# Optimization experiments

Measured on AMD Instinct MI355X. Metric: run time of the kernel, lower is better.

Reference implementation:

```python
import jax, jax.numpy as jnp
import numpy as np

B, S, H, NH = 2, 2048, 1024, 16
HD = H // NH  # head_dim = 64


def setup_inputs() -> dict:
    key = jax.random.key(0)
    k1, k2, k3, k4, k5 = jax.random.split(key, 5)
    hidden_states = jax.random.normal(k1, (B, S, H), dtype=jnp.float32)
    # additive causal mask: 0 on/below diagonal, -1e9 above
    causal = jnp.tril(jnp.ones((S, S), dtype=jnp.bool_))
    attention_mask = jnp.where(causal, 0.0, -1e9).astype(jnp.float32)[None, None, :, :]
    scale = 0.02
    Wq = jax.random.normal(k2, (H, H), dtype=jnp.float32) * scale
    Wk = jax.random.normal(k3, (H, H), dtype=jnp.float32) * scale
    Wv = jax.random.normal(k4, (H, H), dtype=jnp.float32) * scale
    Wo = jax.random.normal(k5, (H, H), dtype=jnp.float32) * scale
    return {"hidden_states": hidden_states, "attention_mask": attention_mask,
            "Wq": Wq, "Wk": Wk, "Wv": Wv, "Wo": Wo}


def reference(hidden_states, attention_mask, Wq, Wk, Wv, Wo):
    b, s, _ = hidden_states.shape
    # nn.Linear: y = x @ W.T
    q = (hidden_states @ Wq.T).reshape(b, s, NH, HD).transpose(0, 2, 1, 3)  # [B,NH,S,HD]
    k = (hidden_states @ Wk.T).reshape(b, s, NH, HD).transpose(0, 2, 1, 3)
    v = (hidden_states @ Wv.T).reshape(b, s, NH, HD).transpose(0, 2, 1, 3)
    scores = jnp.einsum('bhqd,bhkd->bhqk', q, k) / jnp.sqrt(jnp.float32(HD))
    scores = scores + attention_mask
    attn = jax.nn.softmax(scores, axis=-1)
    out = jnp.einsum('bhqk,bhkd->bhqd', attn, v)  # [B,NH,S,HD]
    out = out.transpose(0, 2, 1, 3).reshape(b, s, H)
    return out @ Wo.T
```

## Files before the change

kernel.cpp:

```cpp
#include <hip/hip_runtime.h>
#include <hip/hip_bf16.h>

#define B_   2
#define S_   2048
#define H_   1024
#define NH_  16
#define HD_  64
#define MTOT 4096
#define KD   1024

typedef __attribute__((ext_vector_type(4)))  float    f32x4;
typedef __attribute__((ext_vector_type(16))) float    f32x16;
typedef __attribute__((ext_vector_type(8)))  short    bf16x8;
typedef __attribute__((ext_vector_type(4)))  short    bf16x4;
typedef __attribute__((ext_vector_type(2)))  unsigned u32x2;
typedef __attribute__((ext_vector_type(4)))  unsigned u32x4;

__device__ inline short f2bf(float x) {
    union { float f; unsigned u; } v; v.f = x;
    unsigned r = v.u + 0x7fffu + ((v.u >> 16) & 1u);
    return (short)(r >> 16);
}
__device__ inline unsigned pk2(float lo, float hi) {
    return (unsigned)(unsigned short)f2bf(lo) | ((unsigned)(unsigned short)f2bf(hi) << 16);
}
__device__ inline unsigned cvtpk(float lo, float hi) {
    unsigned r;
    asm("v_cvt_pk_bf16_f32 %0, %1, %2" : "=v"(r) : "v"(lo), "v"(hi));
    return r;
}
__device__ inline float max3f(float a, float b, float c) {
    float r;
    asm("v_max3_f32 %0, %1, %2, %3" : "=v"(r) : "v"(a), "v"(b), "v"(c));
    return r;
}
__device__ inline void gload16(const void* g, void* l) {
    __builtin_amdgcn_global_load_lds(
        (const __attribute__((address_space(1))) unsigned*)g,
        (__attribute__((address_space(3))) unsigned*)l, 16, 0, 0);
}

__global__ __launch_bounds__(256) void cvt_x(const float* __restrict__ x,
                                             unsigned* __restrict__ xb) {
    const size_t i = ((size_t)blockIdx.x * 256 + threadIdx.x) * 8;
    const f32x4 a = *(const f32x4*)(x + i);
    const f32x4 b = *(const f32x4*)(x + i + 4);
    u32x4 p;
    p[0] = pk2(a[0], a[1]); p[1] = pk2(a[2], a[3]);
    p[2] = pk2(b[0], b[1]); p[3] = pk2(b[2], b[3]);
    *(u32x4*)(xb + i / 2) = p;
}

__global__ __launch_bounds__(256) void wcvt(const float* __restrict__ W0,
                                            const float* __restrict__ W1,
                                            const float* __restrict__ W2,
                                            const float* __restrict__ W3,
                                            unsigned* __restrict__ wb) {
    const float* W = (blockIdx.y == 0) ? W0 : (blockIdx.y == 1) ? W1
                   : (blockIdx.y == 2) ? W2 : W3;
    const size_t i = ((size_t)blockIdx.x * 256 + threadIdx.x) * 8;
    const f32x4 a = *(const f32x4*)(W + i);
    const f32x4 b = *(const f32x4*)(W + i + 4);
    u32x4 p;
    p[0] = pk2(a[0], a[1]); p[1] = pk2(a[2], a[3]);
    p[2] = pk2(b[0], b[1]); p[3] = pk2(b[2], b[3]);
    *(u32x4*)(wb + (size_t)blockIdx.y * (H_ * KD / 2) + i / 2) = p;
}

template <int MODE>
__global__ __launch_bounds__(256) void gemm_m97(const short* __restrict__ A,
                                                const short* __restrict__ Wb,
                                                short* __restrict__ outb,
                                                float* __restrict__ outf) {
    __shared__ short Sm[128 * 128];
    short* As = Sm;
    short* Bs = Sm + 8192;

    const int tid = threadIdx.x, wave = tid >> 6, lane = tid & 63;
    const int wm = (wave >> 1) * 64, wn = (wave & 1) * 64;
    const int m0 = blockIdx.x * 128;

    int n0, widx;
    if constexpr (MODE == 0) {
        widx = blockIdx.y >> 3;
        n0 = (blockIdx.y & 7) * 128;
    } else {
        widx = 0;
        n0 = blockIdx.y * 128;
    }
    const short* W = Wb + (size_t)widx * H_ * KD;

    f32x4 acc[4][4] = {};

    for (int k0 = 0; k0 < KD; k0 += 64) {
#pragma unroll
        for (int c = 0; c < 4; ++c) {
            const int lin = wave * 4096 + c * 1024 + lane * 16;
            const int row = lin >> 7;
            const int col = (lin & 127) ^ ((row & 7) << 4);
            gload16(A + (size_t)(m0 + row) * KD + k0 + (col >> 1),
                    (char*)As + wave * 4096 + c * 1024);
            gload16(W + (size_t)(n0 + row) * KD + k0 + (col >> 1),
                    (char*)Bs + wave * 4096 + c * 1024);
        }
        __syncthreads();

#pragma unroll
        for (int ks = 0; ks < 2; ++ks) {
            bf16x8 af[4], bf[4];
#pragma unroll
            for (int i = 0; i < 4; ++i) {
                const int row = wm + i * 16 + (lane & 15);
                af[i] = *(const bf16x8*)((char*)As + row * 128 +
                        ((ks * 64 + (lane >> 4) * 16) ^ ((row & 7) << 4)));
            }
#pragma unroll
            for (int j = 0; j < 4; ++j) {
                const int row = wn + j * 16 + (lane & 15);
                bf[j] = *(const bf16x8*)((char*)Bs + row * 128 +
                        ((ks * 64 + (lane >> 4) * 16) ^ ((row & 7) << 4)));
            }
#pragma unroll
            for (int i = 0; i < 4; ++i)
#pragma unroll
                for (int j = 0; j < 4; ++j)
                    acc[i][j] = __builtin_amdgcn_mfma_f32_16x16x32_bf16(af[i], bf[j], acc[i][j], 0, 0, 0);
        }
        __syncthreads();
    }

    if constexpr (MODE == 0) {
        if (widx == 2) {
#pragma unroll
            for (int i = 0; i < 4; ++i)
#pragma unroll
                for (int j = 0; j < 4; ++j) {
                    const int mi2 = (wm + i * 16 + (lane >> 4) * 4) * 2;
                    const int ni  = wn + j * 16 + (lane & 15);
                    bf16x4 w;
#pragma unroll
                    for (int r = 0; r < 4; ++r) w[r] = f2bf(acc[i][j][r]);
                    *(bf16x4*)((char*)Sm + ((ni * 256 + mi2) ^ ((ni & 7) << 4))) = w;
                }
            __syncthreads();
            const int d = tid >> 1, shalf = tid & 1;
            const int bb = m0 >> 11, sbase = (m0 & 2047) + shalf * 64;
            const int hd = (n0 + d) >> 6, dd = (n0 + d) & 63;
            short* dst = outb + (size_t)2 * MTOT * H_ +
                         (((size_t)(bb * NH_ + hd)) * HD_ + dd) * S_ + sbase;
#pragma unroll
            for (int k = 0; k < 8; ++k) {
                const int byt = (d * 256 + shalf * 128 + k * 16) ^ ((d & 7) << 4);
                *(bf16x8*)(dst + k * 8) = *(const bf16x8*)((char*)Sm + byt);
            }
        } else {
#pragma unroll
            for (int i = 0; i < 4; ++i)
#pragma unroll
                for (int j = 0; j < 4; ++j)
#pragma unroll
                    for (int r = 0; r < 4; ++r) {
                        const int mi = wm + i * 16 + (lane >> 4) * 4 + r;
                        const int ni = wn + j * 16 + (lane & 15);
                        const int byt = (mi * 256 + ni * 2) ^ ((mi & 7) << 4);
                        *(short*)((char*)Sm + byt) = f2bf(acc[i][j][r]);
                    }
            __syncthreads();
            const int row = tid >> 1, half = tid & 1;
            const int m = m0 + row, bb = m >> 11, s = m & 2047;
            const int hh = (n0 >> 6) + half;
            short* dst = outb + (size_t)widx * MTOT * H_ +
                         (((size_t)(bb * NH_ + hh)) * S_ + s) * HD_;
#pragma unroll
            for (int k = 0; k < 8; ++k) {
                const int byt = (row * 256 + half * 128 + k * 16) ^ ((row & 7) << 4);
                *(bf16x8*)(dst + k * 8) = *(const bf16x8*)((char*)Sm + byt);
            }
        }
    } else {
#pragma unroll
        for (int i = 0; i < 4; ++i)
#pragma unroll
            for (int j = 0; j < 4; ++j)
#pragma unroll
                for (int r = 0; r < 4; ++r) {
                    const int m = m0 + wm + i * 16 + (lane >> 4) * 4 + r;
                    const int n = n0 + wn + j * 16 + (lane & 15);
                    outf[(size_t)m * H_ + n] = acc[i][j][r];
                }
    }
}

__global__ __launch_bounds__(128, 4) void flash8(const short* __restrict__ Qb,
                                                 const short* __restrict__ Kb,
                                                 const short* __restrict__ Vtb,
                                                 short* __restrict__ Ob) {
    const int u = blockIdx.x;
    const int qu = 63 - (u >> 5);
    const int bh = u & 31;
    const int b = bh >> 4, h = bh & 15;

    const int tid = threadIdx.x, par = tid >> 6, lane = tid & 63;
    const int qw0 = qu * 32;
    const size_t hoff = ((size_t)(b * NH_ + h)) * S_ * HD_;
    const short* Q  = Qb  + hoff;
    const short* K  = Kb  + hoff;
    const short* Vt = Vtb + hoff;

    const int ql = lane & 31;
    const int hh = lane >> 5;

    bf16x8 qf[4];
#pragma unroll
    for (int ds = 0; ds < 4; ++ds)
        qf[ds] = *(const bf16x8*)(Q + (size_t)(qw0 + ql) * HD_ + ds * 16 + hh * 8);

    f32x16 ot[2] = {};
    float mrun = -1e30f, lrun = 0.f;
    const float c2 = 0.18033688011112042f;

    const int niter = (qw0 + 95) >> 6;
    for (int kt = par; kt < niter; kt += 2) {
        bf16x8 kf[2][4];
#pragma unroll
        for (int t = 0; t < 2; ++t)
#pragma unroll
            for (int ds = 0; ds < 4; ++ds)
                kf[t][ds] = *(const bf16x8*)(K + (size_t)(kt * 64 + t * 32 + ql) * HD_ +
                                             ds * 16 + hh * 8);

        f32x16 st[2] = {};
        __builtin_amdgcn_s_setprio(1);
#pragma unroll
        for (int t = 0; t < 2; ++t)
#pragma unroll
            for (int ds = 0; ds < 4; ++ds)
                st[t] = __builtin_amdgcn_mfma_f32_32x32x16_bf16(kf[t][ds], qf[ds], st[t], 0, 0, 0);
        __builtin_amdgcn_s_setprio(0);

        bf16x8 vf[2][4];
#pragma unroll
        for (int dt = 0; dt < 2; ++dt)
#pragma unroll
            for (int ks = 0; ks < 4; ++ks)
                vf[dt][ks] = *(const bf16x8*)(Vt + (size_t)(dt * 32 + ql) * S_ +
                                              kt * 64 + ks * 16 + hh * 8);

        const bool need_mask = (kt * 64 + 63) > qw0;
        float sraw[32];
#pragma unroll
        for (int t = 0; t < 2; ++t)
#pragma unroll
            for (int r = 0; r < 16; ++r) {
                float v = st[t][r];
                if (need_mask) {
                    const int key = kt * 64 + t * 32 + (r & 3) + 8 * (r >> 2) + 4 * hh;
                    if (key > qw0 + ql) v = -1e30f;
                }
                sraw[t * 16 + r] = v;
            }

        float ma = fmaxf(sraw[0], sraw[1]);
        float mb = fmaxf(sraw[2], sraw[3]);
#pragma unroll
        for (int i = 4; i < 32; i += 4) {
            ma = max3f(ma, sraw[i],     sraw[i + 1]);
            mb = max3f(mb, sraw[i + 2], sraw[i + 3]);
        }
        const float pmax = fmaxf(fmaxf(ma, mb), __shfl_xor(fmaxf(ma, mb), 32, 64));

        if (!__all((pmax - mrun) <= 44.36f)) {
            const float mnew = fmaxf(mrun, pmax);
            const float corr = exp2f((mrun - mnew) * c2);
            mrun = mnew;
            lrun *= corr;
#pragma unroll
            for (int dt = 0; dt < 2; ++dt)
#pragma unroll
                for (int r = 0; r < 16; ++r) ot[dt][r] *= corr;
        }
        const float mc = mrun * c2;

        float p[32];
#pragma unroll
        for (int i = 0; i < 32; ++i) p[i] = exp2f(fmaf(sraw[i], c2, -mc));
        float ts[16];
#pragma unroll
        for (int i = 0; i < 16; ++i) ts[i] = p[i] + p[i + 16];
#pragma unroll
        for (int stp = 8; stp >= 1; stp >>= 1)
#pragma unroll
            for (int i = 0; i < 8; ++i)
                if (i < stp) ts[i] += ts[i + stp];
        lrun += ts[0] + __shfl_xor(ts[0], 32, 64);

#pragma unroll
        for (int ks = 0; ks < 4; ++ks) {
            const int t = ks >> 1, rb = (ks & 1) * 8;
            const unsigned a0 = cvtpk(p[t * 16 + rb + 0], p[t * 16 + rb + 1]);
            const unsigned a1 = cvtpk(p[t * 16 + rb + 2], p[t * 16 + rb + 3]);
            const unsigned a2 = cvtpk(p[t * 16 + rb + 4], p[t * 16 + rb + 5]);
            const unsigned a3 = cvtpk(p[t * 16 + rb + 6], p[t * 16 + rb + 7]);
            const unsigned s0 = __shfl_xor(a0, 32, 64);
            const unsigned s1 = __shfl_xor(a1, 32, 64);
            const unsigned s2 = __shfl_xor(a2, 32, 64);
            const unsigned s3 = __shfl_xor(a3, 32, 64);
            u32x4 pw;
            pw[0] = hh ? s2 : a0;
            pw[1] = hh ? s3 : a1;
            pw[2] = hh ? a2 : s0;
            pw[3] = hh ? a3 : s1;
            const bf16x8 pf = __builtin_bit_cast(bf16x8, pw);
            __builtin_amdgcn_s_setprio(1);
#pragma unroll
            for (int dt = 0; dt < 2; ++dt)
                ot[dt] = __builtin_amdgcn_mfma_f32_32x32x16_bf16(vf[dt][ks], pf, ot[dt], 0, 0, 0);
            __builtin_amdgcn_s_setprio(0);
        }
    }

    __shared__ float Osh[64][36];
    __shared__ float Msh[64][2];

    if (par == 1) {
#pragma unroll
        for (int dt = 0; dt < 2; ++dt)
#pragma unroll
            for (int g4 = 0; g4 < 4; ++g4) {
                f32x4 t;
                t[0] = ot[dt][g4 * 4 + 0]; t[1] = ot[dt][g4 * 4 + 1];
                t[2] = ot[dt][g4 * 4 + 2]; t[3] = ot[dt][g4 * 4 + 3];
                *(f32x4*)(&Osh[lane][dt * 16 + g4 * 4]) = t;
            }
        Msh[lane][0] = mrun;
        Msh[lane][1] = lrun;
    }
    __syncthreads();

    if (par == 0) {
        const float mB = Msh[lane][0];
        const float lB = Msh[lane][1];
        const float m  = fmaxf(mrun, mB);
        const float al = exp2f((mrun - m) * c2);
        const float be = exp2f((mB - m) * c2);
        const float inv = 1.f / (al * lrun + be * lB);
        const float ai = al * inv, bi = be * inv;

        short* orow = Ob + ((size_t)(b * S_) + qw0 + ql) * H_ + h * HD_;
#pragma unroll
        for (int dt = 0; dt < 2; ++dt)
#pragma unroll
            for (int g4 = 0; g4 < 4; ++g4) {
                const f32x4 ob = *(const f32x4*)(&Osh[lane][dt * 16 + g4 * 4]);
                const int dbase = dt * 32 + 8 * g4 + 4 * hh;
                u32x2 w;
                w[0] = cvtpk(ot[dt][g4 * 4 + 0] * ai + ob[0] * bi,
                             ot[dt][g4 * 4 + 1] * ai + ob[1] * bi);
                w[1] = cvtpk(ot[dt][g4 * 4 + 2] * ai + ob[2] * bi,
                             ot[dt][g4 * 4 + 3] * ai + ob[3] * bi);
                *(u32x2*)(orow + dbase) = w;
            }
    }
}

extern "C" void kernel_launch(void* const* d_in, const int* in_sizes, int n_in,
                              void* d_out, int out_size, void* d_ws, size_t ws_size,
                              hipStream_t stream) {
    const float* x  = (const float*)d_in[0];
    const float* Wq = (const float*)d_in[2];
    const float* Wk = (const float*)d_in[3];
    const float* Wv = (const float*)d_in[4];
    const float* Wo = (const float*)d_in[5];
    float* out = (float*)d_out;

    short* qkv = (short*)d_ws;
    short* xb  = qkv + (size_t)3 * MTOT * H_;
    short* wb  = xb + (size_t)MTOT * H_;

    cvt_x<<<2048, 256, 0, stream>>>(x, (unsigned*)xb);
    wcvt<<<dim3(512, 4), 256, 0, stream>>>(Wq, Wk, Wv, Wo, (unsigned*)wb);

    gemm_m97<0><<<dim3(32, 24), 256, 0, stream>>>(xb, wb, qkv, nullptr);

    flash8<<<dim3(2048), 128, 0, stream>>>(
        qkv, qkv + (size_t)MTOT * H_, qkv + (size_t)2 * MTOT * H_, xb);

    gemm_m97<1><<<dim3(32, 8), 256, 0, stream>>>(
        xb, wb + (size_t)3 * H_ * KD, nullptr, out);
}
```

Measured before the change: 180.9 us.

## Split attention KV parity across blocks and merge partials in separate kernel

The flash kernel now gives each block four 32-row query groups (256 threads) for one KV parity, instead of two waves of one block splitting the KV range. Each block writes unnormalized fp32 partial outputs plus running max and sum to workspace, and a new merge kernel combines the two parities and writes the bf16 attention output. This removes the in-block LDS exchange and barrier and aims to raise occupancy and balance, at the cost of extra global traffic (about 32 MB of fp32 partials) and one more kernel launch.

```diff
diff --git a/kernel.cpp b/kernel.cpp
--- a/kernel.cpp
+++ b/kernel.cpp
@@ -8,6 +8,7 @@
 #define HD_  64
 #define MTOT 4096
 #define KD   1024
+#define NROW 65536
 
 typedef __attribute__((ext_vector_type(4)))  float    f32x4;
 typedef __attribute__((ext_vector_type(16))) float    f32x16;
@@ -15,6 +16,7 @@
 typedef __attribute__((ext_vector_type(4)))  short    bf16x4;
 typedef __attribute__((ext_vector_type(2)))  unsigned u32x2;
 typedef __attribute__((ext_vector_type(4)))  unsigned u32x4;
+typedef __attribute__((ext_vector_type(2)))  float    f32x2;
 
 __device__ inline short f2bf(float x) {
     union { float f; unsigned u; } v; v.f = x;
@@ -191,17 +193,19 @@
     }
 }
 
-__global__ __launch_bounds__(128, 4) void flash8(const short* __restrict__ Qb,
+__global__ __launch_bounds__(256, 3) void flash9(const short* __restrict__ Qb,
                                                  const short* __restrict__ Kb,
                                                  const short* __restrict__ Vtb,
-                                                 short* __restrict__ Ob) {
-    const int u = blockIdx.x;
-    const int qu = 63 - (u >> 5);
-    const int bh = u & 31;
-    const int b = bh >> 4, h = bh & 15;
-
-    const int tid = threadIdx.x, par = tid >> 6, lane = tid & 63;
-    const int qw0 = qu * 32;
+                                                 float* __restrict__ Op,
+                                                 float* __restrict__ Ml) {
+    const int bx = blockIdx.x;
+    const int qt = 15 - (bx >> 6);
+    const int rem = bx & 63;
+    const int h = rem >> 2, b = (rem >> 1) & 1, par = rem & 1;
+
+    const int tid = threadIdx.x, qg = tid >> 6, lane = tid & 63;
+    const int q0 = qt * 128;
+    const int qw0 = q0 + qg * 32;
     const size_t hoff = ((size_t)(b * NH_ + h)) * S_ * HD_;
     const short* Q  = Qb  + hoff;
     const short* K  = Kb  + hoff;
@@ -219,8 +223,8 @@
     float mrun = -1e30f, lrun = 0.f;
     const float c2 = 0.18033688011112042f;
 
-    const int niter = (qw0 + 95) >> 6;
-    for (int kt = par; kt < niter; kt += 2) {
+    const int wniter = ((qw0 + 31) >> 6) + 1;
+    for (int kt = par; kt < wniter; kt += 2) {
         bf16x8 kf[2][4];
 #pragma unroll
         for (int t = 0; t < 2; ++t)
@@ -319,47 +323,50 @@
         }
     }
 
-    __shared__ float Osh[64][36];
-    __shared__ float Msh[64][2];
-
-    if (par == 1) {
-#pragma unroll
-        for (int dt = 0; dt < 2; ++dt)
-#pragma unroll
-            for (int g4 = 0; g4 < 4; ++g4) {
-                f32x4 t;
-                t[0] = ot[dt][g4 * 4 + 0]; t[1] = ot[dt][g4 * 4 + 1];
-                t[2] = ot[dt][g4 * 4 + 2]; t[3] = ot[dt][g4 * 4 + 3];
-                *(f32x4*)(&Osh[lane][dt * 16 + g4 * 4]) = t;
-            }
-        Msh[lane][0] = mrun;
-        Msh[lane][1] = lrun;
-    }
-    __syncthreads();
-
-    if (par == 0) {
-        const float mB = Msh[lane][0];
-        const float lB = Msh[lane][1];
-        const float m  = fmaxf(mrun, mB);
-        const float al = exp2f((mrun - m) * c2);
-        const float be = exp2f((mB - m) * c2);
-        const float inv = 1.f / (al * lrun + be * lB);
-        const float ai = al * inv, bi = be * inv;
-
-        short* orow = Ob + ((size_t)(b * S_) + qw0 + ql) * H_ + h * HD_;
-#pragma unroll
-        for (int dt = 0; dt < 2; ++dt)
-#pragma unroll
-            for (int g4 = 0; g4 < 4; ++g4) {
-                const f32x4 ob = *(const f32x4*)(&Osh[lane][dt * 16 + g4 * 4]);
-                const int dbase = dt * 32 + 8 * g4 + 4 * hh;
-                u32x2 w;
-                w[0] = cvtpk(ot[dt][g4 * 4 + 0] * ai + ob[0] * bi,
-                             ot[dt][g4 * 4 + 1] * ai + ob[1] * bi);
-                w[1] = cvtpk(ot[dt][g4 * 4 + 2] * ai + ob[2] * bi,
-                             ot[dt][g4 * 4 + 3] * ai + ob[3] * bi);
-                *(u32x2*)(orow + dbase) = w;
-            }
+    const int rowid = (b * NH_ + h) * S_ + qw0 + ql;
+    float* dst = Op + (size_t)par * ((size_t)NROW * HD_) + (size_t)rowid * HD_;
+#pragma unroll
+    for (int dt = 0; dt < 2; ++dt)
+#pragma unroll
+        for (int g4 = 0; g4 < 4; ++g4) {
+            f32x4 t;
+            t[0] = ot[dt][g4 * 4 + 0]; t[1] = ot[dt][g4 * 4 + 1];
+            t[2] = ot[dt][g4 * 4 + 2]; t[3] = ot[dt][g4 * 4 + 3];
+            *(f32x4*)(dst + dt * 32 + 8 * g4 + 4 * hh) = t;
+        }
+    if (hh == 0) {
+        f32x2 ml; ml[0] = mrun; ml[1] = lrun;
+        *(f32x2*)(Ml + ((size_t)par * NROW + rowid) * 2) = ml;
+    }
+}
+
+__global__ __launch_bounds__(256) void attn_merge(const float* __restrict__ Op,
+                                                  const float* __restrict__ Ml,
+                                                  short* __restrict__ Ob) {
+    const int gid = blockIdx.x * 256 + threadIdx.x;
+    const int row = gid >> 2, seg = gid & 3;
+    const float m0 = Ml[(size_t)row * 2 + 0], l0 = Ml[(size_t)row * 2 + 1];
+    const float m1 = Ml[((size_t)NROW + row) * 2 + 0], l1 = Ml[((size_t)NROW + row) * 2 + 1];
+    const float c2 = 0.18033688011112042f;
+    const float m  = fmaxf(m0, m1);
+    const float a  = exp2f((m0 - m) * c2);
+    const float be = exp2f((m1 - m) * c2);
+    const float inv = 1.f / (a * l0 + be * l1);
+    const float ai = a * inv, bi = be * inv;
+
+    const float* p0 = Op + (size_t)row * HD_ + seg * 16;
+    const float* p1 = Op + (size_t)NROW * HD_ + (size_t)row * HD_ + seg * 16;
+    const int b = row >> 15, h = (row >> 11) & 15, s = row & 2047;
+    short* dstp = Ob + ((size_t)(b * S_ + s)) * H_ + h * HD_ + seg * 16;
+
+#pragma unroll
+    for (int q = 0; q < 4; ++q) {
+        const f32x4 x0 = *(const f32x4*)(p0 + q * 4);
+        const f32x4 x1 = *(const f32x4*)(p1 + q * 4);
+        u32x2 w;
+        w[0] = cvtpk(x0[0] * ai + x1[0] * bi, x0[1] * ai + x1[1] * bi);
+        w[1] = cvtpk(x0[2] * ai + x1[2] * bi, x0[3] * ai + x1[3] * bi);
+        *(u32x2*)(dstp + q * 4) = w;
     }
 }
 
@@ -376,14 +383,17 @@
     short* qkv = (short*)d_ws;
     short* xb  = qkv + (size_t)3 * MTOT * H_;
     short* wb  = xb + (size_t)MTOT * H_;
+    float* Op  = (float*)(wb + (size_t)4 * H_ * KD);
+    float* Ml  = Op + (size_t)2 * NROW * HD_;
 
     cvt_x<<<2048, 256, 0, stream>>>(x, (unsigned*)xb);
     wcvt<<<dim3(512, 4), 256, 0, stream>>>(Wq, Wk, Wv, Wo, (unsigned*)wb);
 
     gemm_m97<0><<<dim3(32, 24), 256, 0, stream>>>(xb, wb, qkv, nullptr);
 
-    flash8<<<dim3(2048), 128, 0, stream>>>(
-        qkv, qkv + (size_t)MTOT * H_, qkv + (size_t)2 * MTOT * H_, xb);
+    flash9<<<dim3(1024), 256, 0, stream>>>(
+        qkv, qkv + (size_t)MTOT * H_, qkv + (size_t)2 * MTOT * H_, Op, Ml);
+    attn_merge<<<dim3(1024), 256, 0, stream>>>(Op, Ml, xb);
 
     gemm_m97<1><<<dim3(32, 8), 256, 0, stream>>>(
         xb, wb + (size_t)3 * H_ * KD, nullptr, out);
```

New measurement: 161.7 us. 1.12x faster.
